# Performance work log

Measured on AMD Instinct MI355X. Metric: run time of the kernel, lower is better.

## Reference

```python
import jax, jax.numpy as jnp
import numpy as np

B, C, H, W = 8, 64, 64, 64
R = 4
INTER = C // R   # 16
QK = C // 8      # 8
OUT = 64
EPS = 1e-5

def _bn(h, s, b, m, v):
    # inference-mode BatchNorm2d over channel dim of NCHW
    inv = s / jnp.sqrt(v + EPS)
    return h * inv[None, :, None, None] + (b - m * inv)[None, :, None, None]

def _conv1x1(h, w, b):
    # 1x1 conv == per-pixel matmul over channels
    return jnp.einsum('oc,bchw->bohw', w, h) + b[None, :, None, None]

def setup_inputs() -> dict:
    key = jax.random.key(0)
    ks = jax.random.split(key, 16)
    def wgt(k, shape):
        return jax.random.normal(k, shape, jnp.float32) * 0.05
    ones = lambda n: jnp.ones((n,), jnp.float32)
    zeros = lambda n: jnp.zeros((n,), jnp.float32)
    return {
        'x': jax.random.normal(ks[0], (B, C, H, W), jnp.float32),
        'lw1': wgt(ks[1], (INTER, C)), 'lb1': zeros(INTER),
        'ls1': ones(INTER), 'lbb1': zeros(INTER), 'lm1': zeros(INTER), 'lv1': ones(INTER),
        'lw2': wgt(ks[2], (C, INTER)), 'lb2': zeros(C),
        'ls2': ones(C), 'lbb2': zeros(C), 'lm2': zeros(C), 'lv2': ones(C),
        'gw1': wgt(ks[3], (INTER, C)), 'gb1': zeros(INTER),
        'gs1': ones(INTER), 'gbb1': zeros(INTER), 'gm1': zeros(INTER), 'gv1': ones(INTER),
        'gw2': wgt(ks[4], (C, INTER)), 'gb2': zeros(C),
        'gs2': ones(C), 'gbb2': zeros(C), 'gm2': zeros(C), 'gv2': ones(C),
        'qw': wgt(ks[5], (QK, C)), 'qb': zeros(QK),
        'kw': wgt(ks[6], (QK, C)), 'kb': zeros(QK),
        'vw': wgt(ks[7], (C, C)), 'vb': zeros(C),
        'gamma': jnp.zeros((1,), jnp.float32),  # torch init: zeros
        'cw': wgt(ks[8], (OUT, C, 3, 3)), 'cb': zeros(OUT),
        'cs': ones(OUT), 'cbb': zeros(OUT), 'cm': zeros(OUT), 'cv': ones(OUT),
    }

def reference(x, lw1, lb1, ls1, lbb1, lm1, lv1, lw2, lb2, ls2, lbb2, lm2, lv2,
              gw1, gb1, gs1, gbb1, gm1, gv1, gw2, gb2, gs2, gbb2, gm2, gv2,
              qw, qb, kw, kb, vw, vb, gamma, cw, cb, cs, cbb, cm, cv):
    # --- SE-style channel gating: local branch (per-pixel) + global branch (GAP) ---
    xl = _bn(_conv1x1(jax.nn.relu(_bn(_conv1x1(x, lw1, lb1), ls1, lbb1, lm1, lv1)), lw2, lb2),
             ls2, lbb2, lm2, lv2)
    g = x.mean(axis=(2, 3), keepdims=True)  # AdaptiveAvgPool2d(1) -> [B,C,1,1]
    xg = _bn(_conv1x1(jax.nn.relu(_bn(_conv1x1(g, gw1, gb1), gs1, gbb1, gm1, gv1)), gw2, gb2),
             gs2, gbb2, gm2, gv2)
    xo = x * jax.nn.sigmoid(xl + xg)
    # --- full spatial self-attention (bmm -> softmax -> bmm, unscaled) ---
    # NOTE: the original forward computes this, forms gamma*out + xo, then
    # immediately overwrites `out` with conv(xo); we reproduce that faithfully.
    b_, c_, h_, w_ = x.shape
    n = h_ * w_
    q = _conv1x1(x, qw, qb).reshape(b_, QK, n)
    k = _conv1x1(x, kw, kb).reshape(b_, QK, n)
    att = jax.nn.softmax(jnp.einsum('bcn,bcm->bnm', q, k), axis=-1)  # [B,N,N]
    v = _conv1x1(x, vw, vb).reshape(b_, c_, n)
    attn_out = jnp.einsum('bcm,bnm->bcn', v, att).reshape(b_, c_, h_, w_)
    _dead = gamma[0] * attn_out + xo  # discarded by original module
    # --- final 3x3 conv + BN + ReLU applied to the gated features xo ---
    y = jax.lax.conv_general_dilated(xo, cw, (1, 1), 'SAME',
                                     dimension_numbers=('NCHW', 'OIHW', 'NCHW'))
    y = y + cb[None, :, None, None]
    return jax.nn.relu(_bn(y, cs, cbb, cm, cv))
```

## Files before the change

### kernel.cpp

```cpp
#include <hip/hip_runtime.h>
#include <hip/hip_bf16.h>

#define NPIX 4096
#define FEPS 1e-5f

typedef __hip_bfloat16 bf16;
typedef __attribute__((ext_vector_type(8))) short bf16x8;
typedef __attribute__((ext_vector_type(4))) float f32x4;

#define OFF_FOLD 64
#define OFF_G    512
#define OFF_LW1  1024
#define OFF_LW2  2048
#define OFF_GW1  3072
#define OFF_GW2  4096
#define WSWZ_BYTES_OFF 20480
#define XO_BYTES_OFF   94208

template<typename T> __device__ __forceinline__ float ldf(const T* p);
template<> __device__ __forceinline__ float ldf<bf16>(const bf16* p)  { return __bfloat162float(*p); }
template<> __device__ __forceinline__ float ldf<float>(const float* p){ return *p; }

template<typename T> __device__ __forceinline__ void stf(T* p, float v);
template<> __device__ __forceinline__ void stf<bf16>(bf16* p, float v)  { *p = __float2bfloat16(v); }
template<> __device__ __forceinline__ void stf<float>(float* p, float v){ *p = v; }

__device__ __forceinline__ unsigned short f2bu(float f) {
    union { bf16 h; unsigned short u; } c; c.h = __float2bfloat16(f); return c.u;
}
__device__ __forceinline__ float blo(unsigned u) {
    union { unsigned i; float f; } c; c.i = u << 16; return c.f;
}
__device__ __forceinline__ float bhi(unsigned u) {
    union { unsigned i; float f; } c; c.i = u & 0xffff0000u; return c.f;
}

__device__ __forceinline__ int probe_flag(const unsigned* __restrict__ x,
                                          int tid, int* sflag)
{
    if (tid < 64) {
        unsigned w = x[tid];
        unsigned h = w & 0xffffu;
        int e = (int)((h >> 7) & 0xff);
        int hit = (h == 0u || (e >= 96 && e <= 160)) ? 1 : 2;
        hit = (hit == 1) ? 1 : 0;
        unsigned long long m = __ballot(hit);
        if (tid == 0) *sflag = (__popcll(m) >= 40) ? 1 : 2;
    }
    __syncthreads();
    return *sflag;
}

struct PrepArgs7 { const void* p[30]; };

template<typename T>
__device__ void prep_body(const PrepArgs7& a, float* __restrict__ ws,
                          unsigned short* __restrict__ wswz, int flag)
{
    const T* lw1  = (const T*)a.p[0];  const T* lb1  = (const T*)a.p[1];
    const T* ls1  = (const T*)a.p[2];  const T* lbb1 = (const T*)a.p[3];
    const T* lm1  = (const T*)a.p[4];  const T* lv1  = (const T*)a.p[5];
    const T* lw2  = (const T*)a.p[6];  const T* lb2  = (const T*)a.p[7];
    const T* ls2  = (const T*)a.p[8];  const T* lbb2 = (const T*)a.p[9];
    const T* lm2  = (const T*)a.p[10]; const T* lv2  = (const T*)a.p[11];
    const T* gw1  = (const T*)a.p[12]; const T* gb1  = (const T*)a.p[13];
    const T* gs1  = (const T*)a.p[14]; const T* gbb1 = (const T*)a.p[15];
    const T* gm1  = (const T*)a.p[16]; const T* gv1  = (const T*)a.p[17];
    const T* gw2  = (const T*)a.p[18]; const T* gb2  = (const T*)a.p[19];
    const T* gs2  = (const T*)a.p[20]; const T* gbb2 = (const T*)a.p[21];
    const T* gm2  = (const T*)a.p[22]; const T* gv2  = (const T*)a.p[23];
    const T* cw   = (const T*)a.p[24]; const T* cb   = (const T*)a.p[25];
    const T* cs   = (const T*)a.p[26]; const T* cbb  = (const T*)a.p[27];
    const T* cm   = (const T*)a.p[28]; const T* cv   = (const T*)a.p[29];

    int bx = blockIdx.x;
    int tid = threadIdx.x;
    if (bx < 16) {
        for (int e = tid; e < 2304; e += 256) {
            int E = bx * 2304 + e;
            int j = E & 7;
            int F = E >> 3;
            int l = F & 63;
            int g = (F >> 6) & 3;
            int ts = F >> 8;
            int s = ts & 1;
            int t = ts >> 1;
            int oc = g * 16 + (l & 15);
            int ic = s * 32 + (l >> 4) * 8 + j;
            wswz[E] = f2bu(ldf(cw + (oc * 64 + ic) * 9 + t));
        }
    } else if (bx == 16) {
        for (int e = tid; e < 4096; e += 256) {
            if (e < 1024)      ws[OFF_LW1 + e]        = ldf(lw1 + e);
            else if (e < 2048) ws[OFF_LW2 + e - 1024] = ldf(lw2 + e - 1024);
            else if (e < 3072) ws[OFF_GW1 + e - 2048] = ldf(gw1 + e - 2048);
            else               ws[OFF_GW2 + e - 3072] = ldf(gw2 + e - 3072);
        }
    } else {
        if (tid == 0) ((int*)ws)[0] = flag;
        if (tid < 16) {
            float inv = ldf(ls1 + tid) * rsqrtf(ldf(lv1 + tid) + FEPS);
            ws[OFF_FOLD + 0  + tid] = inv;
            ws[OFF_FOLD + 16 + tid] = ldf(lb1 + tid) * inv + ldf(lbb1 + tid) - ldf(lm1 + tid) * inv;
            float ginv = ldf(gs1 + tid) * rsqrtf(ldf(gv1 + tid) + FEPS);
            ws[OFF_FOLD + 160 + tid] = ginv;
            ws[OFF_FOLD + 176 + tid] = ldf(gb1 + tid) * ginv + ldf(gbb1 + tid) - ldf(gm1 + tid) * ginv;
        }
        if (tid < 64) {
            float inv2 = ldf(ls2 + tid) * rsqrtf(ldf(lv2 + tid) + FEPS);
            ws[OFF_FOLD + 32 + tid] = inv2;
            ws[OFF_FOLD + 96 + tid] = ldf(lb2 + tid) * inv2 + ldf(lbb2 + tid) - ldf(lm2 + tid) * inv2;
            float ginv2 = ldf(gs2 + tid) * rsqrtf(ldf(gv2 + tid) + FEPS);
            ws[OFF_FOLD + 192 + tid] = ginv2;
            ws[OFF_FOLD + 256 + tid] = ldf(gb2 + tid) * ginv2 + ldf(gbb2 + tid) - ldf(gm2 + tid) * ginv2;
            float cinv = ldf(cs + tid) * rsqrtf(ldf(cv + tid) + FEPS);
            ws[OFF_FOLD + 320 + tid] = cinv;
            ws[OFF_FOLD + 384 + tid] = ldf(cb + tid) * cinv + ldf(cbb + tid) - ldf(cm + tid) * cinv;
        }
    }
}

__global__ void r7_prep_means(PrepArgs7 a, const void* __restrict__ xv,
                              float* __restrict__ ws,
                              unsigned short* __restrict__ wswz)
{
    __shared__ int sflag;
    int t = threadIdx.x;
    int flag = probe_flag((const unsigned*)xv, t, &sflag);
    int bx = blockIdx.x;

    if (bx < 18) {
        if (flag == 1) prep_body<bf16>(a, ws, wswz, flag);
        else           prep_body<float>(a, ws, wswz, flag);
        return;
    }

    int bc = bx - 18;
    float s = 0.f;
    if (flag == 1) {
        const uint4* p = (const uint4*)((const bf16*)xv + (size_t)bc * NPIX);
#pragma unroll
        for (int i = 0; i < 2; ++i) {
            uint4 v = p[t * 2 + i];
            s += blo(v.x) + bhi(v.x) + blo(v.y) + bhi(v.y)
               + blo(v.z) + bhi(v.z) + blo(v.w) + bhi(v.w);
        }
    } else {
        const float4* p = (const float4*)((const float*)xv + (size_t)bc * NPIX);
#pragma unroll
        for (int i = 0; i < 4; ++i) {
            float4 v = p[t * 4 + i];
            s += v.x + v.y + v.z + v.w;
        }
    }
#pragma unroll
    for (int off = 32; off > 0; off >>= 1) s += __shfl_down(s, off, 64);
    __shared__ float red[4];
    if ((t & 63) == 0) red[t >> 6] = s;
    __syncthreads();
    if (t == 0)
        ws[OFF_G + bc] = (red[0] + red[1] + red[2] + red[3]) * (1.0f / 4096.0f);
}

__device__ void gate_slow_f32(const void* __restrict__ xv, float* __restrict__ ws,
                              uint4* __restrict__ xo)
{
    int b = blockIdx.x >> 5;
    int n = (blockIdx.x & 31) * 128 + threadIdx.x;
    int tid = threadIdx.x;

    __shared__ float t1[16];
    __shared__ float xg[64];
    if (tid < 16) {
        float s = 0.f;
#pragma unroll
        for (int c = 0; c < 64; ++c)
            s += ws[OFF_GW1 + tid * 64 + c] * ws[OFF_G + b * 64 + c];
        t1[tid] = fmaxf(ws[OFF_FOLD + 160 + tid] * s + ws[OFF_FOLD + 176 + tid], 0.f);
    }
    __syncthreads();
    if (tid < 64) {
        float s = 0.f;
#pragma unroll
        for (int j = 0; j < 16; ++j) s += ws[OFF_GW2 + tid * 16 + j] * t1[j];
        xg[tid] = ws[OFF_FOLD + 192 + tid] * s + ws[OFF_FOLD + 256 + tid];
    }
    __syncthreads();

    const float* xb = (const float*)xv + (size_t)b * 64 * NPIX + n;
    float xr[64];
#pragma unroll
    for (int c = 0; c < 64; ++c) xr[c] = xb[c * NPIX];

    float h[16];
#pragma unroll
    for (int i = 0; i < 16; ++i) {
        float s = 0.f;
#pragma unroll
        for (int c = 0; c < 64; ++c) s += ws[OFF_LW1 + i * 64 + c] * xr[c];
        h[i] = fmaxf(ws[OFF_FOLD + 0 + i] * s + ws[OFF_FOLD + 16 + i], 0.f);
    }

    uint4* xop = xo + ((size_t)b * NPIX + n) * 8;
#pragma unroll
    for (int cg = 0; cg < 8; ++cg) {
        unsigned v[8];
#pragma unroll
        for (int j = 0; j < 8; ++j) {
            int c = cg * 8 + j;
            float s = 0.f;
#pragma unroll
            for (int k = 0; k < 16; ++k) s += ws[OFF_LW2 + c * 16 + k] * h[k];
            float z = ws[OFF_FOLD + 32 + c] * s + ws[OFF_FOLD + 96 + c] + xg[c];
            v[j] = (unsigned)f2bu(xr[c] / (1.0f + __expf(-z)));
        }
        uint4 pk;
        pk.x = v[0] | (v[1] << 16);
        pk.y = v[2] | (v[3] << 16);
        pk.z = v[4] | (v[5] << 16);
        pk.w = v[6] | (v[7] << 16);
        xop[cg] = pk;
    }
}

__global__ __launch_bounds__(128)
void r7_gate(const void* __restrict__ xv, float* __restrict__ ws,
             uint4* __restrict__ xo)
{
    if (((const int*)ws)[0] != 1) { gate_slow_f32(xv, ws, xo); return; }

    int bx = blockIdx.x;
    int b = bx >> 5;
    int pix0 = (bx & 31) * 128;
    int t = threadIdx.x;

    __shared__ float t1[16];
    __shared__ float xg[64];
    __shared__ char tile[64 * 256];

    const uint4* xsrc = (const uint4*)((const bf16*)xv + (size_t)b * 64 * NPIX + pix0);
    uint4 ld[8];
#pragma unroll
    for (int k = 0; k < 8; ++k) {
        int e = k * 128 + t;
        int c = e >> 4;
        int u = e & 15;
        ld[k] = xsrc[(size_t)c * 512 + u];
    }
    if (t < 16) {
        float s = 0.f;
#pragma unroll
        for (int c = 0; c < 64; ++c)
            s += ws[OFF_GW1 + t * 64 + c] * ws[OFF_G + b * 64 + c];
        t1[t] = fmaxf(ws[OFF_FOLD + 160 + t] * s + ws[OFF_FOLD + 176 + t], 0.f);
    }
#pragma unroll
    for (int k = 0; k < 8; ++k) {
        int e = k * 128 + t;
        int c = e >> 4;
        int u = e & 15;
        *(uint4*)(tile + c * 256 + u * 16) = ld[k];
    }
    __syncthreads();
    if (t < 64) {
        float s = 0.f;
#pragma unroll
        for (int j = 0; j < 16; ++j) s += ws[OFF_GW2 + t * 16 + j] * t1[j];
        xg[t] = ws[OFF_FOLD + 192 + t] * s + ws[OFF_FOLD + 256 + t];
    }
    float xr[64];
#pragma unroll
    for (int c = 0; c < 64; ++c)
        xr[c] = __bfloat162float(*(const bf16*)(tile + c * 256 + t * 2));
    float h[16];
#pragma unroll
    for (int i = 0; i < 16; ++i) {
        float s = 0.f;
#pragma unroll
        for (int c = 0; c < 64; ++c) s += ws[OFF_LW1 + i * 64 + c] * xr[c];
        h[i] = fmaxf(ws[OFF_FOLD + 0 + i] * s + ws[OFF_FOLD + 16 + i], 0.f);
    }
    __syncthreads();
#pragma unroll
    for (int cg = 0; cg < 8; ++cg) {
        unsigned v[8];
#pragma unroll
        for (int j = 0; j < 8; ++j) {
            int c = cg * 8 + j;
            float s = 0.f;
#pragma unroll
            for (int k = 0; k < 16; ++k) s += ws[OFF_LW2 + c * 16 + k] * h[k];
            float z = ws[OFF_FOLD + 32 + c] * s + ws[OFF_FOLD + 96 + c] + xg[c];
            v[j] = (unsigned)f2bu(xr[c] / (1.0f + __expf(-z)));
        }
        uint4 pk;
        pk.x = v[0] | (v[1] << 16);
        pk.y = v[2] | (v[3] << 16);
        pk.z = v[4] | (v[5] << 16);
        pk.w = v[6] | (v[7] << 16);
        *(uint4*)(tile + ((t * 128 + cg * 16) ^ ((t & 7) << 4))) = pk;
    }
    __syncthreads();
    uint4* xop = xo + ((size_t)b * NPIX + pix0) * 8;
#pragma unroll
    for (int k = 0; k < 8; ++k) {
        int e = k * 128 + t;
        int p = e >> 3;
        int u = e & 7;
        xop[e] = *(const uint4*)(tile + ((p * 128 + u * 16) ^ ((p & 7) << 4)));
    }
}

#define CONV_LDS_BYTES (3 * 34 * 128)

template<typename T>
__device__ void conv_body(const bf16x8* __restrict__ wsw, const float* __restrict__ ws,
                          const char* __restrict__ xob_base, void* __restrict__ outv,
                          char* __restrict__ lds)
{
    int bx  = blockIdx.x;
    int b   = bx >> 7;
    int r   = (bx >> 1) & 63;
    int c0  = (bx & 1) * 32;
    int tid = threadIdx.x;
    int w   = tid >> 6;
    int l   = tid & 63;
    int a   = l & 15;
    int q   = l >> 4;

    const char* xob = xob_base + (size_t)b * NPIX * 128;

    for (int e = tid; e < 816; e += 128) {
        int row = e / 272;
        int rm  = e - row * 272;
        int px  = rm >> 3;
        int u   = rm & 7;
        int col = c0 - 1 + px;
        int rr  = r - 1 + row;
        uint4 v = {0u, 0u, 0u, 0u};
        if (col >= 0 && col <= 63) {
            int rc = min(63, max(0, rr));
            v = *(const uint4*)(xob + rc * 8192 + col * 128 + u * 16);
        }
        int byt = ((row * 34 + px) * 128 + u * 16) ^ ((px & 7) << 4);
        *(uint4*)(lds + byt) = v;
    }
    __syncthreads();

    f32x4 acc[2][2] = {};

#pragma unroll
    for (int t = 0; t < 9; ++t) {
        const int dr  = t / 3 - 1;
        const int dci = t % 3;
        int rr = r + dr;
        if (rr < 0 || rr > 63) continue;
        const char* rowp = lds + (dr + 1) * (34 * 128);
#pragma unroll
        for (int s = 0; s < 2; ++s) {
            bf16x8 A0 = wsw[((t * 2 + s) * 4 + 2 * w + 0) * 64 + l];
            bf16x8 A1 = wsw[((t * 2 + s) * 4 + 2 * w + 1) * 64 + l];
            int sq = s * 64 + q * 16;
#pragma unroll
            for (int nf = 0; nf < 2; ++nf) {
                int tp  = nf * 16 + a + dci;
                int byt = tp * 128 + (sq ^ ((tp & 7) << 4));
                bf16x8 B = *(const bf16x8*)(rowp + byt);
                acc[0][nf] = __builtin_amdgcn_mfma_f32_16x16x32_bf16(A0, B, acc[0][nf], 0, 0, 0);
                acc[1][nf] = __builtin_amdgcn_mfma_f32_16x16x32_bf16(A1, B, acc[1][nf], 0, 0, 0);
            }
        }
    }

    const float* cA = ws + OFF_FOLD + 320;
    const float* cB = ws + OFF_FOLD + 384;
    int pixBase = r * 64 + c0;
#pragma unroll
    for (int gi = 0; gi < 2; ++gi) {
        int g = 2 * w + gi;
#pragma unroll
        for (int reg = 0; reg < 4; ++reg) {
            int oc = g * 16 + q * 4 + reg;
            float Af = cA[oc];
            float Bf = cB[oc];
#pragma unroll
            for (int nf = 0; nf < 2; ++nf) {
                int pix = pixBase + nf * 16 + a;
                float y = fmaxf(acc[gi][nf][reg] * Af + Bf, 0.f);
                stf((T*)outv + ((size_t)b * 64 + oc) * NPIX + pix, y);
            }
        }
    }
}

__global__ __launch_bounds__(128)
void r7_conv(const bf16x8* __restrict__ wsw, const float* __restrict__ ws,
             const char* __restrict__ xob_base, void* __restrict__ outv)
{
    __shared__ char lds[CONV_LDS_BYTES];
    if (((const int*)ws)[0] == 1) conv_body<bf16>(wsw, ws, xob_base, outv, lds);
    else                          conv_body<float>(wsw, ws, xob_base, outv, lds);
}

extern "C" void kernel_launch(void* const* d_in, const int* in_sizes, int n_in,
                              void* d_out, int out_size, void* d_ws, size_t ws_size,
                              hipStream_t stream)
{
    (void)in_sizes; (void)n_in; (void)out_size; (void)ws_size;
    const void* x = d_in[0];
    float* ws = (float*)d_ws;
    unsigned short* wswz = (unsigned short*)((char*)d_ws + WSWZ_BYTES_OFF);
    char* xo = (char*)d_ws + XO_BYTES_OFF;

    PrepArgs7 pa;
    for (int i = 0; i < 24; ++i) pa.p[i] = d_in[1 + i];
    for (int i = 0; i < 6; ++i)  pa.p[24 + i] = d_in[32 + i];

    r7_prep_means<<<dim3(530), dim3(256), 0, stream>>>(pa, x, ws, wswz);
    r7_gate<<<dim3(256), dim3(128), 0, stream>>>(x, ws, (uint4*)xo);
    r7_conv<<<dim3(1024), dim3(128), 0, stream>>>(
        (const bf16x8*)wswz, ws, xo, d_out);
}
```

Measured before the change: 177.6 us.

## Split gate channel work across four threads per pixel with LDS-staged weights

The gate kernel now runs 512 threads per block, with four threads per pixel each handling 16 channels. The first 1x1-conv partial sums are reduced with cross-lane shuffles. LW2 is stored transposed, and both local weight matrices are staged in LDS. The input tile uses a padded stride, and the output goes straight to global memory without the swizzled LDS round trip. The goal is to cut per-thread register pressure (xr drops from 64 to 16 values) and raise occupancy. In exchange it adds shuffles and makes each thread recompute the full h vector.

```diff
diff --git a/kernel.cpp b/kernel.cpp
--- a/kernel.cpp
+++ b/kernel.cpp
@@ -42,8 +42,7 @@
         unsigned w = x[tid];
         unsigned h = w & 0xffffu;
         int e = (int)((h >> 7) & 0xff);
-        int hit = (h == 0u || (e >= 96 && e <= 160)) ? 1 : 2;
-        hit = (hit == 1) ? 1 : 0;
+        int hit = (h == 0u || (e >= 96 && e <= 160)) ? 1 : 0;
         unsigned long long m = __ballot(hit);
         if (tid == 0) *sflag = (__popcll(m) >= 40) ? 1 : 2;
     }
@@ -92,7 +91,12 @@
     } else if (bx == 16) {
         for (int e = tid; e < 4096; e += 256) {
             if (e < 1024)      ws[OFF_LW1 + e]        = ldf(lw1 + e);
-            else if (e < 2048) ws[OFF_LW2 + e - 1024] = ldf(lw2 + e - 1024);
+            else if (e < 2048) {
+                int F = e - 1024;
+                int c = F >> 4;
+                int k = F & 15;
+                ws[OFF_LW2 + k * 64 + c] = ldf(lw2 + F);
+            }
             else if (e < 3072) ws[OFF_GW1 + e - 2048] = ldf(gw1 + e - 2048);
             else               ws[OFF_GW2 + e - 3072] = ldf(gw2 + e - 3072);
         }
@@ -120,7 +124,7 @@
     }
 }
 
-__global__ void r7_prep_means(PrepArgs7 a, const void* __restrict__ xv,
+__global__ void r8_prep_means(PrepArgs7 a, const void* __restrict__ xv,
                               float* __restrict__ ws,
                               unsigned short* __restrict__ wswz)
 {
@@ -166,8 +170,8 @@
                               uint4* __restrict__ xo)
 {
     int b = blockIdx.x >> 5;
-    int n = (blockIdx.x & 31) * 128 + threadIdx.x;
     int tid = threadIdx.x;
+    int n = (blockIdx.x & 31) * 128 + tid;
 
     __shared__ float t1[16];
     __shared__ float xg[64];
@@ -186,6 +190,7 @@
         xg[tid] = ws[OFF_FOLD + 192 + tid] * s + ws[OFF_FOLD + 256 + tid];
     }
     __syncthreads();
+    if (tid >= 128) return;
 
     const float* xb = (const float*)xv + (size_t)b * 64 * NPIX + n;
     float xr[64];
@@ -210,7 +215,7 @@
             int c = cg * 8 + j;
             float s = 0.f;
 #pragma unroll
-            for (int k = 0; k < 16; ++k) s += ws[OFF_LW2 + c * 16 + k] * h[k];
+            for (int k = 0; k < 16; ++k) s += ws[OFF_LW2 + k * 64 + c] * h[k];
             float z = ws[OFF_FOLD + 32 + c] * s + ws[OFF_FOLD + 96 + c] + xg[c];
             v[j] = (unsigned)f2bu(xr[c] / (1.0f + __expf(-z)));
         }
@@ -223,8 +228,10 @@
     }
 }
 
-__global__ __launch_bounds__(128)
-void r7_gate(const void* __restrict__ xv, float* __restrict__ ws,
+#define TSTRIDE 67
+
+__global__ __launch_bounds__(512)
+void r8_gate(const void* __restrict__ xv, float* __restrict__ ws,
              uint4* __restrict__ xo)
 {
     if (((const int*)ws)[0] != 1) { gate_slow_f32(xv, ws, xo); return; }
@@ -233,16 +240,20 @@
     int b = bx >> 5;
     int pix0 = (bx & 31) * 128;
     int t = threadIdx.x;
-
+    int p   = t >> 2;
+    int sub = t & 3;
+
+    __shared__ unsigned tile32[64 * TSTRIDE];
+    __shared__ float w1s[1024];
+    __shared__ float w2s[1024];
     __shared__ float t1[16];
     __shared__ float xg[64];
-    __shared__ char tile[64 * 256];
 
     const uint4* xsrc = (const uint4*)((const bf16*)xv + (size_t)b * 64 * NPIX + pix0);
-    uint4 ld[8];
-#pragma unroll
-    for (int k = 0; k < 8; ++k) {
-        int e = k * 128 + t;
+    uint4 ld[2];
+#pragma unroll
+    for (int k = 0; k < 2; ++k) {
+        int e = k * 512 + t;
         int c = e >> 4;
         int u = e & 15;
         ld[k] = xsrc[(size_t)c * 512 + u];
@@ -255,11 +266,17 @@
         t1[t] = fmaxf(ws[OFF_FOLD + 160 + t] * s + ws[OFF_FOLD + 176 + t], 0.f);
     }
 #pragma unroll
-    for (int k = 0; k < 8; ++k) {
-        int e = k * 128 + t;
+    for (int k = 0; k < 2; ++k) {
+        w1s[k * 512 + t] = ws[OFF_LW1 + k * 512 + t];
+        w2s[k * 512 + t] = ws[OFF_LW2 + k * 512 + t];
+    }
+#pragma unroll
+    for (int k = 0; k < 2; ++k) {
+        int e = k * 512 + t;
         int c = e >> 4;
         int u = e & 15;
-        *(uint4*)(tile + c * 256 + u * 16) = ld[k];
+        unsigned* dst = tile32 + c * TSTRIDE + u * 4;
+        dst[0] = ld[k].x; dst[1] = ld[k].y; dst[2] = ld[k].z; dst[3] = ld[k].w;
     }
     __syncthreads();
     if (t < 64) {
@@ -268,46 +285,45 @@
         for (int j = 0; j < 16; ++j) s += ws[OFF_GW2 + t * 16 + j] * t1[j];
         xg[t] = ws[OFF_FOLD + 192 + t] * s + ws[OFF_FOLD + 256 + t];
     }
-    float xr[64];
-#pragma unroll
-    for (int c = 0; c < 64; ++c)
-        xr[c] = __bfloat162float(*(const bf16*)(tile + c * 256 + t * 2));
+    const char* tb = (const char*)tile32;
+    float xr[16];
+#pragma unroll
+    for (int j = 0; j < 16; ++j) {
+        int c = sub * 16 + j;
+        xr[j] = __bfloat162float(*(const bf16*)(tb + c * 268 + p * 2));
+    }
     float h[16];
 #pragma unroll
     for (int i = 0; i < 16; ++i) {
         float s = 0.f;
 #pragma unroll
-        for (int c = 0; c < 64; ++c) s += ws[OFF_LW1 + i * 64 + c] * xr[c];
+        for (int j = 0; j < 16; ++j)
+            s += w1s[i * 64 + sub * 16 + j] * xr[j];
+        s += __shfl_xor(s, 1, 64);
+        s += __shfl_xor(s, 2, 64);
         h[i] = fmaxf(ws[OFF_FOLD + 0 + i] * s + ws[OFF_FOLD + 16 + i], 0.f);
     }
     __syncthreads();
-#pragma unroll
-    for (int cg = 0; cg < 8; ++cg) {
+    uint4* xop = xo + ((size_t)b * NPIX + pix0 + p) * 8 + sub * 2;
+#pragma unroll
+    for (int jg = 0; jg < 2; ++jg) {
         unsigned v[8];
 #pragma unroll
-        for (int j = 0; j < 8; ++j) {
-            int c = cg * 8 + j;
+        for (int j2 = 0; j2 < 8; ++j2) {
+            int j = jg * 8 + j2;
+            int c = sub * 16 + j;
             float s = 0.f;
 #pragma unroll
-            for (int k = 0; k < 16; ++k) s += ws[OFF_LW2 + c * 16 + k] * h[k];
+            for (int k = 0; k < 16; ++k) s += w2s[k * 64 + c] * h[k];
             float z = ws[OFF_FOLD + 32 + c] * s + ws[OFF_FOLD + 96 + c] + xg[c];
-            v[j] = (unsigned)f2bu(xr[c] / (1.0f + __expf(-z)));
+            v[j2] = (unsigned)f2bu(xr[j] / (1.0f + __expf(-z)));
         }
         uint4 pk;
         pk.x = v[0] | (v[1] << 16);
         pk.y = v[2] | (v[3] << 16);
         pk.z = v[4] | (v[5] << 16);
         pk.w = v[6] | (v[7] << 16);
-        *(uint4*)(tile + ((t * 128 + cg * 16) ^ ((t & 7) << 4))) = pk;
-    }
-    __syncthreads();
-    uint4* xop = xo + ((size_t)b * NPIX + pix0) * 8;
-#pragma unroll
-    for (int k = 0; k < 8; ++k) {
-        int e = k * 128 + t;
-        int p = e >> 3;
-        int u = e & 7;
-        xop[e] = *(const uint4*)(tile + ((p * 128 + u * 16) ^ ((p & 7) << 4)));
+        xop[jg] = pk;
     }
 }
 
@@ -394,7 +410,7 @@
 }
 
 __global__ __launch_bounds__(128)
-void r7_conv(const bf16x8* __restrict__ wsw, const float* __restrict__ ws,
+void r8_conv(const bf16x8* __restrict__ wsw, const float* __restrict__ ws,
              const char* __restrict__ xob_base, void* __restrict__ outv)
 {
     __shared__ char lds[CONV_LDS_BYTES];
@@ -416,8 +432,8 @@
     for (int i = 0; i < 24; ++i) pa.p[i] = d_in[1 + i];
     for (int i = 0; i < 6; ++i)  pa.p[24 + i] = d_in[32 + i];
 
-    r7_prep_means<<<dim3(530), dim3(256), 0, stream>>>(pa, x, ws, wswz);
-    r7_gate<<<dim3(256), dim3(128), 0, stream>>>(x, ws, (uint4*)xo);
-    r7_conv<<<dim3(1024), dim3(128), 0, stream>>>(
+    r8_prep_means<<<dim3(530), dim3(256), 0, stream>>>(pa, x, ws, wswz);
+    r8_gate<<<dim3(256), dim3(512), 0, stream>>>(x, ws, (uint4*)xo);
+    r8_conv<<<dim3(1024), dim3(128), 0, stream>>>(
         (const bf16x8*)wswz, ws, xo, d_out);
 }
```

New measurement: 214.5 us. 20.8% more time.

## Compute local gate branch with bf16 MFMA and double gate grid size

Applied to the files above, without the earlier changes.

The gate kernel's per-pixel local branch (64->16->64 1x1 convs) is moved from scalar FP32 loops to bf16 MFMA instructions, using weight fragments prepared by a new prep block. The LDS transpose tile is dropped: x is gathered straight from global memory and xo is written directly in the channel-last layout the conv expects. The grid grows from 256 to 512 blocks of 64 pixels each to raise parallelism. This costs some precision, since the hidden activation is rounded to bf16, and adds strided 2-byte global loads, including a second read of x for the final multiply.

```diff
diff --git a/kernel.cpp b/kernel.cpp
--- a/kernel.cpp
+++ b/kernel.cpp
@@ -6,7 +6,10 @@
 
 typedef __hip_bfloat16 bf16;
 typedef __attribute__((ext_vector_type(8))) short bf16x8;
+typedef __attribute__((ext_vector_type(4))) short bf16x4;
 typedef __attribute__((ext_vector_type(4))) float f32x4;
+
+#define MFMA16(A,B,C) __builtin_amdgcn_mfma_f32_16x16x16bf16_1k(A,B,C,0,0,0)
 
 #define OFF_FOLD 64
 #define OFF_G    512
@@ -16,6 +19,7 @@
 #define OFF_GW2  4096
 #define WSWZ_BYTES_OFF 20480
 #define XO_BYTES_OFF   94208
+#define GWF_BYTES_OFF  4288512
 
 template<typename T> __device__ __forceinline__ float ldf(const T* p);
 template<> __device__ __forceinline__ float ldf<bf16>(const bf16* p)  { return __bfloat162float(*p); }
@@ -27,6 +31,9 @@
 
 __device__ __forceinline__ unsigned short f2bu(float f) {
     union { bf16 h; unsigned short u; } c; c.h = __float2bfloat16(f); return c.u;
+}
+__device__ __forceinline__ float bu2f(unsigned short u) {
+    union { unsigned i; float f; } c; c.i = ((unsigned)u) << 16; return c.f;
 }
 __device__ __forceinline__ float blo(unsigned u) {
     union { unsigned i; float f; } c; c.i = u << 16; return c.f;
@@ -42,8 +49,7 @@
         unsigned w = x[tid];
         unsigned h = w & 0xffffu;
         int e = (int)((h >> 7) & 0xff);
-        int hit = (h == 0u || (e >= 96 && e <= 160)) ? 1 : 2;
-        hit = (hit == 1) ? 1 : 0;
+        int hit = (h == 0u || (e >= 96 && e <= 160)) ? 1 : 0;
         unsigned long long m = __ballot(hit);
         if (tid == 0) *sflag = (__popcll(m) >= 40) ? 1 : 2;
     }
@@ -55,7 +61,8 @@
 
 template<typename T>
 __device__ void prep_body(const PrepArgs7& a, float* __restrict__ ws,
-                          unsigned short* __restrict__ wswz, int flag)
+                          unsigned short* __restrict__ wswz,
+                          unsigned short* __restrict__ gwf, int flag)
 {
     const T* lw1  = (const T*)a.p[0];  const T* lb1  = (const T*)a.p[1];
     const T* ls1  = (const T*)a.p[2];  const T* lbb1 = (const T*)a.p[3];
@@ -92,11 +99,16 @@
     } else if (bx == 16) {
         for (int e = tid; e < 4096; e += 256) {
             if (e < 1024)      ws[OFF_LW1 + e]        = ldf(lw1 + e);
-            else if (e < 2048) ws[OFF_LW2 + e - 1024] = ldf(lw2 + e - 1024);
+            else if (e < 2048) {
+                int F = e - 1024;
+                int c = F >> 4;
+                int k = F & 15;
+                ws[OFF_LW2 + k * 64 + c] = ldf(lw2 + F);
+            }
             else if (e < 3072) ws[OFF_GW1 + e - 2048] = ldf(gw1 + e - 2048);
             else               ws[OFF_GW2 + e - 3072] = ldf(gw2 + e - 3072);
         }
-    } else {
+    } else if (bx == 17) {
         if (tid == 0) ((int*)ws)[0] = flag;
         if (tid < 16) {
             float inv = ldf(ls1 + tid) * rsqrtf(ldf(lv1 + tid) + FEPS);
@@ -117,25 +129,41 @@
             ws[OFF_FOLD + 320 + tid] = cinv;
             ws[OFF_FOLD + 384 + tid] = ldf(cb + tid) * cinv + ldf(cbb + tid) - ldf(cm + tid) * cinv;
         }
-    }
-}
-
-__global__ void r7_prep_means(PrepArgs7 a, const void* __restrict__ xv,
+    } else {
+        for (int e = tid; e < 2048; e += 256) {
+            if (e < 1024) {
+                int j = e & 7;
+                int l = (e >> 3) & 63;
+                int s = e >> 9;
+                gwf[e] = f2bu(ldf(lw1 + (l & 15) * 64 + s * 32 + (l >> 4) * 8 + j));
+            } else {
+                int e2 = e - 1024;
+                int j = e2 & 3;
+                int l = (e2 >> 2) & 63;
+                int g = e2 >> 8;
+                gwf[e] = f2bu(ldf(lw2 + (g * 16 + (l & 15)) * 16 + (l >> 4) * 4 + j));
+            }
+        }
+    }
+}
+
+__global__ void r9_prep_means(PrepArgs7 a, const void* __restrict__ xv,
                               float* __restrict__ ws,
-                              unsigned short* __restrict__ wswz)
+                              unsigned short* __restrict__ wswz,
+                              unsigned short* __restrict__ gwf)
 {
     __shared__ int sflag;
     int t = threadIdx.x;
     int flag = probe_flag((const unsigned*)xv, t, &sflag);
     int bx = blockIdx.x;
 
-    if (bx < 18) {
-        if (flag == 1) prep_body<bf16>(a, ws, wswz, flag);
-        else           prep_body<float>(a, ws, wswz, flag);
+    if (bx < 19) {
+        if (flag == 1) prep_body<bf16>(a, ws, wswz, gwf, flag);
+        else           prep_body<float>(a, ws, wswz, gwf, flag);
         return;
     }
 
-    int bc = bx - 18;
+    int bc = bx - 19;
     float s = 0.f;
     if (flag == 1) {
         const uint4* p = (const uint4*)((const bf16*)xv + (size_t)bc * NPIX);
@@ -165,8 +193,8 @@
 __device__ void gate_slow_f32(const void* __restrict__ xv, float* __restrict__ ws,
                               uint4* __restrict__ xo)
 {
-    int b = blockIdx.x >> 5;
-    int n = (blockIdx.x & 31) * 128 + threadIdx.x;
+    int bx = blockIdx.x;
+    int b = bx >> 6;
     int tid = threadIdx.x;
 
     __shared__ float t1[16];
@@ -186,6 +214,8 @@
         xg[tid] = ws[OFF_FOLD + 192 + tid] * s + ws[OFF_FOLD + 256 + tid];
     }
     __syncthreads();
+    if (tid >= 64) return;
+    int n = (bx & 63) * 64 + tid;
 
     const float* xb = (const float*)xv + (size_t)b * 64 * NPIX + n;
     float xr[64];
@@ -210,7 +240,7 @@
             int c = cg * 8 + j;
             float s = 0.f;
 #pragma unroll
-            for (int k = 0; k < 16; ++k) s += ws[OFF_LW2 + c * 16 + k] * h[k];
+            for (int k = 0; k < 16; ++k) s += ws[OFF_LW2 + k * 64 + c] * h[k];
             float z = ws[OFF_FOLD + 32 + c] * s + ws[OFF_FOLD + 96 + c] + xg[c];
             v[j] = (unsigned)f2bu(xr[c] / (1.0f + __expf(-z)));
         }
@@ -224,90 +254,121 @@
 }
 
 __global__ __launch_bounds__(128)
-void r7_gate(const void* __restrict__ xv, float* __restrict__ ws,
+void r9_gate(const void* __restrict__ xv, float* __restrict__ ws,
              uint4* __restrict__ xo)
 {
     if (((const int*)ws)[0] != 1) { gate_slow_f32(xv, ws, xo); return; }
 
     int bx = blockIdx.x;
-    int b = bx >> 5;
-    int pix0 = (bx & 31) * 128;
-    int t = threadIdx.x;
+    int b   = bx >> 6;
+    int tid = threadIdx.x;
+    int w   = tid >> 6;
+    int l   = tid & 63;
+    int a   = l & 15;
+    int q   = l >> 4;
 
     __shared__ float t1[16];
-    __shared__ float xg[64];
-    __shared__ char tile[64 * 256];
-
-    const uint4* xsrc = (const uint4*)((const bf16*)xv + (size_t)b * 64 * NPIX + pix0);
-    uint4 ld[8];
-#pragma unroll
-    for (int k = 0; k < 8; ++k) {
-        int e = k * 128 + t;
-        int c = e >> 4;
-        int u = e & 15;
-        ld[k] = xsrc[(size_t)c * 512 + u];
-    }
-    if (t < 16) {
+    __shared__ float xgs[64];
+
+    const unsigned short* gwf =
+        (const unsigned short*)((const char*)ws + GWF_BYTES_OFF);
+    bf16x8 W1f0 = ((const bf16x8*)gwf)[l];
+    bf16x8 W1f1 = ((const bf16x8*)gwf)[64 + l];
+    const bf16x4* wf2 = (const bf16x4*)(gwf + 1024);
+    bf16x4 W2f0 = wf2[l];
+    bf16x4 W2f1 = wf2[64 + l];
+    bf16x4 W2f2 = wf2[128 + l];
+    bf16x4 W2f3 = wf2[192 + l];
+
+    float A1v[4], B1v[4];
+#pragma unroll
+    for (int reg = 0; reg < 4; ++reg) {
+        A1v[reg] = ws[OFF_FOLD + 0  + 4 * q + reg];
+        B1v[reg] = ws[OFF_FOLD + 16 + 4 * q + reg];
+    }
+    float A2v[4][4], B2v[4][4];
+#pragma unroll
+    for (int g = 0; g < 4; ++g)
+#pragma unroll
+        for (int reg = 0; reg < 4; ++reg) {
+            int c = g * 16 + 4 * q + reg;
+            A2v[g][reg] = ws[OFF_FOLD + 32 + c];
+            B2v[g][reg] = ws[OFF_FOLD + 96 + c];
+        }
+
+    if (tid < 16) {
         float s = 0.f;
 #pragma unroll
         for (int c = 0; c < 64; ++c)
-            s += ws[OFF_GW1 + t * 64 + c] * ws[OFF_G + b * 64 + c];
-        t1[t] = fmaxf(ws[OFF_FOLD + 160 + t] * s + ws[OFF_FOLD + 176 + t], 0.f);
-    }
-#pragma unroll
-    for (int k = 0; k < 8; ++k) {
-        int e = k * 128 + t;
-        int c = e >> 4;
-        int u = e & 15;
-        *(uint4*)(tile + c * 256 + u * 16) = ld[k];
-    }
-    __syncthreads();
-    if (t < 64) {
+            s += ws[OFF_GW1 + tid * 64 + c] * ws[OFF_G + b * 64 + c];
+        t1[tid] = fmaxf(ws[OFF_FOLD + 160 + tid] * s + ws[OFF_FOLD + 176 + tid], 0.f);
+    }
+    __syncthreads();
+    if (tid < 64) {
         float s = 0.f;
 #pragma unroll
-        for (int j = 0; j < 16; ++j) s += ws[OFF_GW2 + t * 16 + j] * t1[j];
-        xg[t] = ws[OFF_FOLD + 192 + t] * s + ws[OFF_FOLD + 256 + t];
-    }
-    float xr[64];
-#pragma unroll
-    for (int c = 0; c < 64; ++c)
-        xr[c] = __bfloat162float(*(const bf16*)(tile + c * 256 + t * 2));
-    float h[16];
-#pragma unroll
-    for (int i = 0; i < 16; ++i) {
-        float s = 0.f;
-#pragma unroll
-        for (int c = 0; c < 64; ++c) s += ws[OFF_LW1 + i * 64 + c] * xr[c];
-        h[i] = fmaxf(ws[OFF_FOLD + 0 + i] * s + ws[OFF_FOLD + 16 + i], 0.f);
-    }
-    __syncthreads();
-#pragma unroll
-    for (int cg = 0; cg < 8; ++cg) {
-        unsigned v[8];
+        for (int j = 0; j < 16; ++j) s += ws[OFF_GW2 + tid * 16 + j] * t1[j];
+        xgs[tid] = ws[OFF_FOLD + 192 + tid] * s + ws[OFF_FOLD + 256 + tid];
+    }
+    __syncthreads();
+
+    float xgv[4][4];
+#pragma unroll
+    for (int g = 0; g < 4; ++g)
+#pragma unroll
+        for (int reg = 0; reg < 4; ++reg)
+            xgv[g][reg] = xgs[g * 16 + 4 * q + reg];
+
+    const unsigned short* xb = (const unsigned short*)xv + (size_t)b * 64 * NPIX;
+    char* xob = (char*)xo + (size_t)b * NPIX * 128;
+    const f32x4 zz = {0.f, 0.f, 0.f, 0.f};
+    int pxb0 = (bx & 63) * 64 + w * 32;
+
+#pragma unroll
+    for (int tile = 0; tile < 2; ++tile) {
+        int pxl = pxb0 + tile * 16 + a;
+
+        unsigned short g0[8], g1[8];
 #pragma unroll
         for (int j = 0; j < 8; ++j) {
-            int c = cg * 8 + j;
-            float s = 0.f;
-#pragma unroll
-            for (int k = 0; k < 16; ++k) s += ws[OFF_LW2 + c * 16 + k] * h[k];
-            float z = ws[OFF_FOLD + 32 + c] * s + ws[OFF_FOLD + 96 + c] + xg[c];
-            v[j] = (unsigned)f2bu(xr[c] / (1.0f + __expf(-z)));
-        }
-        uint4 pk;
-        pk.x = v[0] | (v[1] << 16);
-        pk.y = v[2] | (v[3] << 16);
-        pk.z = v[4] | (v[5] << 16);
-        pk.w = v[6] | (v[7] << 16);
-        *(uint4*)(tile + ((t * 128 + cg * 16) ^ ((t & 7) << 4))) = pk;
-    }
-    __syncthreads();
-    uint4* xop = xo + ((size_t)b * NPIX + pix0) * 8;
-#pragma unroll
-    for (int k = 0; k < 8; ++k) {
-        int e = k * 128 + t;
-        int p = e >> 3;
-        int u = e & 7;
-        xop[e] = *(const uint4*)(tile + ((p * 128 + u * 16) ^ ((p & 7) << 4)));
+            g0[j] = xb[(q * 8 + j) * NPIX + pxl];
+            g1[j] = xb[(32 + q * 8 + j) * NPIX + pxl];
+        }
+        bf16x8 B0 = { (short)g0[0], (short)g0[1], (short)g0[2], (short)g0[3],
+                      (short)g0[4], (short)g0[5], (short)g0[6], (short)g0[7] };
+        bf16x8 B1 = { (short)g1[0], (short)g1[1], (short)g1[2], (short)g1[3],
+                      (short)g1[4], (short)g1[5], (short)g1[6], (short)g1[7] };
+
+        f32x4 acc = __builtin_amdgcn_mfma_f32_16x16x32_bf16(W1f0, B0, zz, 0, 0, 0);
+        acc = __builtin_amdgcn_mfma_f32_16x16x32_bf16(W1f1, B1, acc, 0, 0, 0);
+
+        bf16x4 Hf = { (short)f2bu(fmaxf(acc[0] * A1v[0] + B1v[0], 0.f)),
+                      (short)f2bu(fmaxf(acc[1] * A1v[1] + B1v[1], 0.f)),
+                      (short)f2bu(fmaxf(acc[2] * A1v[2] + B1v[2], 0.f)),
+                      (short)f2bu(fmaxf(acc[3] * A1v[3] + B1v[3], 0.f)) };
+
+        f32x4 z0 = MFMA16(W2f0, Hf, zz);
+        f32x4 z1 = MFMA16(W2f1, Hf, zz);
+        f32x4 z2 = MFMA16(W2f2, Hf, zz);
+        f32x4 z3 = MFMA16(W2f3, Hf, zz);
+
+        char* rec = xob + (size_t)pxl * 128 + q * 8;
+#pragma unroll
+        for (int g = 0; g < 4; ++g) {
+            const f32x4& zf = (g == 0) ? z0 : (g == 1) ? z1 : (g == 2) ? z2 : z3;
+            unsigned vv[4];
+#pragma unroll
+            for (int reg = 0; reg < 4; ++reg) {
+                int c = g * 16 + 4 * q + reg;
+                float zval = zf[reg] * A2v[g][reg] + B2v[g][reg] + xgv[g][reg];
+                float xval = bu2f(xb[c * NPIX + pxl]);
+                vv[reg] = (unsigned)f2bu(xval / (1.0f + __expf(-zval)));
+            }
+            uint2 pk;
+            pk.x = vv[0] | (vv[1] << 16);
+            pk.y = vv[2] | (vv[3] << 16);
+            *(uint2*)(rec + g * 32) = pk;
+        }
     }
 }
 
@@ -394,7 +455,7 @@
 }
 
 __global__ __launch_bounds__(128)
-void r7_conv(const bf16x8* __restrict__ wsw, const float* __restrict__ ws,
+void r9_conv(const bf16x8* __restrict__ wsw, const float* __restrict__ ws,
              const char* __restrict__ xob_base, void* __restrict__ outv)
 {
     __shared__ char lds[CONV_LDS_BYTES];
@@ -410,14 +471,15 @@
     const void* x = d_in[0];
     float* ws = (float*)d_ws;
     unsigned short* wswz = (unsigned short*)((char*)d_ws + WSWZ_BYTES_OFF);
+    unsigned short* gwf  = (unsigned short*)((char*)d_ws + GWF_BYTES_OFF);
     char* xo = (char*)d_ws + XO_BYTES_OFF;
 
     PrepArgs7 pa;
     for (int i = 0; i < 24; ++i) pa.p[i] = d_in[1 + i];
     for (int i = 0; i < 6; ++i)  pa.p[24 + i] = d_in[32 + i];
 
-    r7_prep_means<<<dim3(530), dim3(256), 0, stream>>>(pa, x, ws, wswz);
-    r7_gate<<<dim3(256), dim3(128), 0, stream>>>(x, ws, (uint4*)xo);
-    r7_conv<<<dim3(1024), dim3(128), 0, stream>>>(
+    r9_prep_means<<<dim3(531), dim3(256), 0, stream>>>(pa, x, ws, wswz, gwf);
+    r9_gate<<<dim3(512), dim3(128), 0, stream>>>(x, ws, (uint4*)xo);
+    r9_conv<<<dim3(1024), dim3(128), 0, stream>>>(
         (const bf16x8*)wswz, ws, xo, d_out);
 }
```

Result: slower. 373.7 us (+110.4%).
